# Kernel optimization log

Measured on AMD Instinct MI355X. Metric: run time of the kernel, lower is better.

The kernel has to match this reference:

```python
import jax, jax.numpy as jnp
import numpy as np

V, E, H, R, RD = 32000, 300, 300, 50, 50  # vocab, word-emb, hidden, rel vocab, rel emb
B, N = 32, 128                            # trees per batch, nodes per tree


def setup_inputs() -> dict:
    key = jax.random.key(0)
    ks = jax.random.split(key, 10)
    root_hidden = jax.random.normal(ks[0], (B, H), jnp.float32)
    relations = jax.random.randint(ks[1], (B, N), 0, R, jnp.int32)
    prev_words = jax.random.randint(ks[2], (B, N), 0, V, jnp.int32)
    # topologically sorted parent pointers: parent[i] in [-1, i-1]; -1 = virtual root
    rng = np.random.default_rng(0)
    parents = np.full((B, N), -1, dtype=np.int32)
    for i in range(1, N):
        parents[:, i] = rng.integers(-1, i, size=B)
    parents = jnp.asarray(parents)
    s_in = 1.0 / np.float32(np.sqrt(RD + E))
    s_h = 1.0 / np.float32(np.sqrt(H))
    emb = jax.random.normal(ks[3], (V, E), jnp.float32) * 0.02
    rel_emb = jax.random.normal(ks[4], (R, RD), jnp.float32) * 0.02
    W_ih = jax.random.normal(ks[5], (4 * H, RD + E), jnp.float32) * s_in
    W_hh = jax.random.normal(ks[6], (4 * H, H), jnp.float32) * s_h
    b_ih = jnp.zeros((4 * H,), jnp.float32)
    b_hh = jnp.zeros((4 * H,), jnp.float32)
    W_out = jax.random.normal(ks[7], (V, H), jnp.float32) * s_h
    b_out = jnp.zeros((V,), jnp.float32)
    return {"root_hidden": root_hidden, "relations": relations, "prev_words": prev_words,
            "parents": parents, "emb": emb, "rel_emb": rel_emb, "W_ih": W_ih, "W_hh": W_hh,
            "b_ih": b_ih, "b_hh": b_hh, "W_out": W_out, "b_out": b_out}


def reference(root_hidden, relations, prev_words, parents, emb, rel_emb,
              W_ih, W_hh, b_ih, b_hh, W_out, b_out):
    # per-node input: rel embedding ++ (teacher-forced) previous word embedding
    x = jnp.concatenate([rel_emb[relations], emb[prev_words]], axis=-1)  # [B,N,RD+E]
    xg = jnp.einsum('bni,gi->bng', x, W_ih) + b_ih                       # [B,N,4H]

    def one_tree(h0, xg_t, pars):
        n = pars.shape[0]
        h_buf = jnp.zeros((n + 1, H), xg_t.dtype).at[0].set(h0)
        c_buf = jnp.zeros((n + 1, H), xg_t.dtype).at[0].set(h0)  # original: hidden=(h,h)

        def step(carry, inp):
            hb, cb = carry
            xg_i, par, idx = inp
            ph = hb[par + 1]
            pc = cb[par + 1]
            gates = xg_i + ph @ W_hh.T + b_hh
            i_g, f_g, g_g, o_g = jnp.split(gates, 4)
            c = jax.nn.sigmoid(f_g) * pc + jax.nn.sigmoid(i_g) * jnp.tanh(g_g)
            h = jax.nn.sigmoid(o_g) * jnp.tanh(c)
            return (hb.at[idx + 1].set(h), cb.at[idx + 1].set(c)), h

        _, hs = jax.lax.scan(step, (h_buf, c_buf), (xg_t, pars, jnp.arange(n)))
        return hs  # [N,H]

    hs = jax.vmap(one_tree)(root_hidden, xg, parents)          # [B,N,H]
    logits = jnp.einsum('bnh,vh->bnv', hs, W_out) + b_out      # [B,N,V]
    return logits
```

## Files before the change

### kernel.cpp

```cpp
#include <hip/hip_runtime.h>
#include <hip/hip_bf16.h>

typedef unsigned short u16;
typedef unsigned int u32;
typedef unsigned long long u64;
typedef __attribute__((ext_vector_type(8))) short short8;
typedef __attribute__((ext_vector_type(4))) float f32x4;

#define NB 32
#define NN 128
#define HH 300
#define NV 32000
#define KP 320
#define KX 352
#define XGS 1280

#define NSLICE 15
#define UPS 20
#define NROWS 80
#define TPBS 320
#define GMAXN 16
#define LDW 328

#define A_LD(p)     __hip_atomic_load((p), __ATOMIC_RELAXED, __HIP_MEMORY_SCOPE_AGENT)
#define A_ST(p, v)  __hip_atomic_store((p), (v), __ATOMIC_RELAXED, __HIP_MEMORY_SCOPE_AGENT)
#define A_ADD(p, v) __hip_atomic_fetch_add((p), (v), __ATOMIC_RELAXED, __HIP_MEMORY_SCOPE_AGENT)

__device__ __forceinline__ float sigm(float x) { return 1.f / (1.f + __expf(-x)); }
__device__ __forceinline__ float tanh_f(float x) {
    float e = __expf(2.f * x);
    return 1.f - 2.f / (e + 1.f);
}
__device__ __forceinline__ u16 f2bf(float f) {
    __hip_bfloat16 b = __float2bfloat16(f);
    return *reinterpret_cast<u16*>(&b);
}

__global__ void k_init(const float* __restrict__ rh, u16* __restrict__ hb16,
                       int* __restrict__ lvl_done) {
    const int stride = gridDim.x * blockDim.x;
    const int idx = blockIdx.x * blockDim.x + threadIdx.x;
    for (int e = idx; e < NB * 129 * 20; e += stride) {
        int row = e / 20, c = 300 + (e - row * 20);
        hb16[(size_t)row * KP + c] = 0;
    }
    for (int e = idx; e < NB * HH; e += stride) {
        int b = e / HH, u = e - b * HH;
        hb16[(size_t)(b * 129) * KP + u] = f2bf(rh[e]);
    }
    for (int e = idx; e < NB * NN; e += stride) lvl_done[e] = 0;
}

__global__ void k_pack(const float* __restrict__ W_ih, const float* __restrict__ W_hh,
                       u16* __restrict__ Wihp, u16* __restrict__ Wp16) {
    const int tot = 1280 * KX + NSLICE * NROWS * LDW;
    for (int n = blockIdx.x * blockDim.x + threadIdx.x; n < tot; n += gridDim.x * blockDim.x) {
        if (n < 1280 * KX) {
            int r = n / KX, k = n - r * KX;
            float v = (r < 1200 && k < 350) ? W_ih[r * 350 + k] : 0.f;
            Wihp[n] = f2bf(v);
        } else {
            int m = n - 1280 * KX;
            int s = m / (NROWS * LDW);
            int rem = m - s * (NROWS * LDW);
            int r = rem / LDW, k = rem - r * LDW;
            int g = r / UPS, ul = r - g * UPS;
            int grow = g * HH + s * UPS + ul;
            float v = (k < HH) ? W_hh[grow * HH + k] : 0.f;
            Wp16[m] = f2bf(v);
        }
    }
}

__global__ void k_gatherX(const int* __restrict__ relations, const int* __restrict__ prev_words,
                          const float* __restrict__ rel_emb, const float* __restrict__ emb,
                          u16* __restrict__ X) {
    for (int e = blockIdx.x * blockDim.x + threadIdx.x; e < NB * NN * KX;
         e += gridDim.x * blockDim.x) {
        int node = e / KX, c = e - node * KX;
        float v = 0.f;
        if (c < 50) v = rel_emb[relations[node] * 50 + c];
        else if (c < 350) v = emb[(size_t)prev_words[node] * 300 + (c - 50)];
        X[e] = f2bf(v);
    }
}

__global__ void k_prep(const int* __restrict__ parents, int* __restrict__ lvl_nodes,
                       int* __restrict__ lvl_cnt, int* __restrict__ lvl_start,
                       int* __restrict__ nlev) {
    __shared__ int dep[NB][NN];
    __shared__ int cnt[NB][NN];
    __shared__ int st[NB][NN];
    const int t = threadIdx.x;
    if (t < NB) {
        for (int l = 0; l < NN; ++l) cnt[t][l] = 0;
        int md = 0;
        for (int i = 0; i < NN; ++i) {
            int p = parents[t * NN + i];
            int d = (p < 0) ? 0 : dep[t][p] + 1;
            dep[t][i] = d;
            cnt[t][d]++;
            md = max(md, d);
        }
        nlev[t] = md + 1;
        int run = 0;
        for (int l = 0; l < NN; ++l) {
            st[t][l] = run;
            lvl_start[t * NN + l] = run;
            lvl_cnt[t * NN + l] = cnt[t][l];
            run += cnt[t][l];
        }
        for (int i = 0; i < NN; ++i) {
            int d = dep[t][i];
            lvl_nodes[t * NN + st[t][d]] = i;
            st[t][d]++;
        }
    }
}

__global__ __launch_bounds__(256) void k_xgemm(const u16* __restrict__ Xbf,
                                               const u16* __restrict__ Wihp,
                                               const float* __restrict__ b_ih,
                                               float* __restrict__ xg) {
    __shared__ __align__(16) u16 As[128 * 40];
    __shared__ __align__(16) u16 Bs[128 * 40];
    const int tid = threadIdx.x;
    const int lane = tid & 63, wv = tid >> 6;
    const int wm = wv >> 1, wn = wv & 1;
    const int mblk = blockIdx.x, nblk = blockIdx.y;
    const u16* Ag = Xbf + (size_t)mblk * 128 * KX;
    const u16* Bg = Wihp + (size_t)nblk * 128 * KX;
    f32x4 acc[4][4] = {};
    const int lrow = lane & 15, lseg = lane >> 4;
    for (int kk = 0; kk < KX; kk += 32) {
#pragma unroll
        for (int q = 0; q < 2; ++q) {
            int s = tid + q * 256;
            int r = s >> 2, seg = s & 3;
            *(uint4*)&As[r * 40 + seg * 8] = *(const uint4*)&Ag[(size_t)r * KX + kk + seg * 8];
            *(uint4*)&Bs[r * 40 + seg * 8] = *(const uint4*)&Bg[(size_t)r * KX + kk + seg * 8];
        }
        __syncthreads();
        short8 av[4], bv[4];
#pragma unroll
        for (int i = 0; i < 4; ++i) {
            av[i] = *(const short8*)&As[(wm * 64 + i * 16 + lrow) * 40 + lseg * 8];
            bv[i] = *(const short8*)&Bs[(wn * 64 + i * 16 + lrow) * 40 + lseg * 8];
        }
#pragma unroll
        for (int i = 0; i < 4; ++i)
#pragma unroll
            for (int j = 0; j < 4; ++j)
                acc[i][j] = __builtin_amdgcn_mfma_f32_16x16x32_bf16(bv[j], av[i], acc[i][j],
                                                                    0, 0, 0);
        __syncthreads();
    }
#pragma unroll
    for (int i = 0; i < 4; ++i) {
        const int row = mblk * 128 + wm * 64 + i * 16 + lrow;
        float* orow = xg + (size_t)row * XGS;
#pragma unroll
        for (int j = 0; j < 4; ++j) {
            const int col = nblk * 128 + wn * 64 + j * 16 + lseg * 4;
            f32x4 v = acc[i][j];
            if (col < 1200) {
                f32x4 bo = *(const f32x4*)&b_ih[col];
                v[0] += bo[0]; v[1] += bo[1]; v[2] += bo[2]; v[3] += bo[3];
            }
            *(f32x4*)&orow[col] = v;
        }
    }
}

__global__ __launch_bounds__(TPBS) void k_scan(const int* __restrict__ parents,
                                               const u16* __restrict__ Wp16,
                                               const float* __restrict__ xg,
                                               const float* __restrict__ b_hh,
                                               const float* __restrict__ rh,
                                               u16* __restrict__ hb16,
                                               const int* __restrict__ lvl_nodes,
                                               const int* __restrict__ lvl_cnt,
                                               const int* __restrict__ lvl_start,
                                               const int* __restrict__ nlev,
                                               int* __restrict__ lvl_done) {
    __shared__ __align__(16) u16 Wl[NROWS * LDW];
    __shared__ __align__(16) u16 hs[GMAXN * LDW];
    __shared__ __align__(16) float gates[GMAXN * 82];
    __shared__ float c_lds[129 * UPS];
    __shared__ int nid_s[GMAXN], par_s[GMAXN];

    const int t = threadIdx.x;
    const int b = blockIdx.x / NSLICE;
    const int s = blockIdx.x % NSLICE;
    const int lane = t & 63, wv = t >> 6;
    const int lrow = lane & 15, lk = lane >> 4;

    {
        const u64* src = (const u64*)(Wp16 + (size_t)s * NROWS * LDW);
        u64* dst = (u64*)Wl;
        for (int e = t; e < NROWS * LDW / 4; e += TPBS) dst[e] = src[e];
    }
    if (t < UPS) c_lds[t] = rh[b * HH + s * UPS + t];
    __syncthreads();

    const int nl = nlev[b];
    for (int l = 0; l < nl; ++l) {
        const int cnt = lvl_cnt[b * NN + l];
        const int start = lvl_start[b * NN + l];
        for (int off = 0; off < cnt; off += GMAXN) {
            const int gc = min(GMAXN, cnt - off);
            if (t < gc) {
                int i = lvl_nodes[b * NN + start + off + t];
                nid_s[t] = i;
                par_s[t] = parents[b * NN + i];
            }
            __syncthreads();
            for (int e = t; e < gc * 80; e += TPBS) {
                const int j = e / 80, q = e - j * 80;
                const u64* hrow = (const u64*)(hb16 +
                    (size_t)(b * 129 + par_s[j] + 1) * KP);
                *(u64*)&hs[j * LDW + q * 4] = A_LD(&hrow[q]);
            }
            __syncthreads();
            {
                f32x4 acc = {};
#pragma unroll
                for (int kk = 0; kk < KP; kk += 32) {
                    short8 av = *(const short8*)&hs[lrow * LDW + kk + lk * 8];
                    short8 bv = *(const short8*)&Wl[(wv * 16 + lrow) * LDW + kk + lk * 8];
                    acc = __builtin_amdgcn_mfma_f32_16x16x32_bf16(av, bv, acc, 0, 0, 0);
                }
#pragma unroll
                for (int r = 0; r < 4; ++r)
                    gates[(lk * 4 + r) * 82 + wv * 16 + lrow] = acc[r];
            }
            __syncthreads();
            if (t < 160) {
                const int j = t / 10, up = t - j * 10;
                if (j < gc) {
                    const int i = nid_s[j];
                    const int par = par_s[j];
                    const int ul0 = up * 2;
                    const float* gj = gates + j * 82;
                    const float* xgp = xg + (size_t)(b * NN + i) * XGS + s * UPS;
                    const float* bhp = b_hh + s * UPS;
                    float hv[2];
#pragma unroll
                    for (int un = 0; un < 2; ++un) {
                        const int ul = ul0 + un;
                        float gs[4];
#pragma unroll
                        for (int g = 0; g < 4; ++g)
                            gs[g] = gj[g * UPS + ul] + xgp[g * HH + ul] + bhp[g * HH + ul];
                        const float pc = c_lds[(par + 1) * UPS + ul];
                        const float cv = sigm(gs[1]) * pc + sigm(gs[0]) * tanh_f(gs[2]);
                        hv[un] = sigm(gs[3]) * tanh_f(cv);
                        c_lds[(i + 1) * UPS + ul] = cv;
                    }
                    const u32 hp = (u32)f2bf(hv[0]) | ((u32)f2bf(hv[1]) << 16);
                    A_ST((u32*)(hb16 + (size_t)(b * 129 + i + 1) * KP + s * UPS + ul0), hp);
                }
            }
            __syncthreads();
        }
        if (l + 1 < nl) {
            if (t == 0) {
                int* dp = &lvl_done[b * NN + l];
                const int old = A_ADD(dp, 1);
                if (old != NSLICE - 1) {
                    while (A_LD(dp) < NSLICE) __builtin_amdgcn_s_sleep(1);
                }
            }
            __syncthreads();
        }
    }
}

__global__ void k_cast_B(const float* __restrict__ W_out, u16* __restrict__ Bm) {
    for (int e = blockIdx.x * blockDim.x + threadIdx.x; e < NV * KP;
         e += gridDim.x * blockDim.x) {
        int v = e / KP, k = e - v * KP;
        float x = (k < HH) ? W_out[v * HH + k] : 0.f;
        Bm[e] = f2bf(x);
    }
}

__global__ __launch_bounds__(256) void k_gemm(const u16* __restrict__ hb16,
                                              const u16* __restrict__ Bbf,
                                              const float* __restrict__ b_out,
                                              float* __restrict__ out) {
    __shared__ __align__(16) u16 As[128 * 40];
    __shared__ __align__(16) u16 Bs[128 * 40];
    const int tid = threadIdx.x;
    const int lane = tid & 63, wv = tid >> 6;
    const int wm = wv >> 1, wn = wv & 1;
    const int bid = blockIdx.x;
    const int newbid = (bid & 7) * 1000 + (bid >> 3);
    const int mblk = newbid & 31, nblk = newbid >> 5;
    const u16* Ag = hb16 + ((size_t)mblk * 129 + 1) * KP;
    const u16* Bg = Bbf + (size_t)nblk * 128 * KP;
    f32x4 acc[4][4] = {};
    const int lrow = lane & 15, lseg = lane >> 4;
    for (int kk = 0; kk < KP; kk += 32) {
#pragma unroll
        for (int q = 0; q < 2; ++q) {
            int s = tid + q * 256;
            int r = s >> 2, seg = s & 3;
            *(uint4*)&As[r * 40 + seg * 8] = *(const uint4*)&Ag[r * KP + kk + seg * 8];
            *(uint4*)&Bs[r * 40 + seg * 8] = *(const uint4*)&Bg[r * KP + kk + seg * 8];
        }
        __syncthreads();
        short8 av[4], bv[4];
#pragma unroll
        for (int i = 0; i < 4; ++i) {
            av[i] = *(const short8*)&As[(wm * 64 + i * 16 + lrow) * 40 + lseg * 8];
            bv[i] = *(const short8*)&Bs[(wn * 64 + i * 16 + lrow) * 40 + lseg * 8];
        }
#pragma unroll
        for (int i = 0; i < 4; ++i)
#pragma unroll
            for (int j = 0; j < 4; ++j)
                acc[i][j] = __builtin_amdgcn_mfma_f32_16x16x32_bf16(bv[j], av[i], acc[i][j],
                                                                    0, 0, 0);
        __syncthreads();
    }
#pragma unroll
    for (int i = 0; i < 4; ++i) {
        const int row = mblk * 128 + wm * 64 + i * 16 + lrow;
        float* orow = out + (size_t)row * NV;
#pragma unroll
        for (int j = 0; j < 4; ++j) {
            const int col = nblk * 128 + wn * 64 + j * 16 + lseg * 4;
            f32x4 v = acc[i][j];
            f32x4 bo = *(const f32x4*)&b_out[col];
            v[0] += bo[0]; v[1] += bo[1]; v[2] += bo[2]; v[3] += bo[3];
            __builtin_nontemporal_store(v, (f32x4*)&orow[col]);
        }
    }
}

extern "C" void kernel_launch(void* const* d_in, const int* in_sizes, int n_in,
                              void* d_out, int out_size, void* d_ws, size_t ws_size,
                              hipStream_t stream) {
    const float* root_hidden = (const float*)d_in[0];
    const int* relations = (const int*)d_in[1];
    const int* prev_words = (const int*)d_in[2];
    const int* parents = (const int*)d_in[3];
    const float* emb = (const float*)d_in[4];
    const float* rel_emb = (const float*)d_in[5];
    const float* W_ih = (const float*)d_in[6];
    const float* W_hh = (const float*)d_in[7];
    const float* b_ih = (const float*)d_in[8];
    const float* b_hh = (const float*)d_in[9];
    const float* W_out = (const float*)d_in[10];
    const float* b_out = (const float*)d_in[11];
    float* out = (float*)d_out;

    float* xg = (float*)d_ws;
    u16* Xbf = (u16*)(xg + 4096 * XGS);
    u16* Wihp = Xbf + 4096 * KX;
    u16* Wp16 = Wihp + 1280 * KX;
    u16* hb16 = Wp16 + NSLICE * NROWS * LDW;
    u16* Bbf = hb16 + 1320960;
    int* lvl_nodes = (int*)(Bbf + 10240000);
    int* lvl_cnt = lvl_nodes + 4096;
    int* lvl_start = lvl_cnt + 4096;
    int* nlev = lvl_start + 4096;
    int* lvl_done = nlev + 64;

    k_init<<<128, 256, 0, stream>>>(root_hidden, hb16, lvl_done);
    k_pack<<<1024, 256, 0, stream>>>(W_ih, W_hh, Wihp, Wp16);
    k_gatherX<<<1024, 256, 0, stream>>>(relations, prev_words, rel_emb, emb, Xbf);
    k_prep<<<1, 64, 0, stream>>>(parents, lvl_nodes, lvl_cnt, lvl_start, nlev);

    k_xgemm<<<dim3(32, 10), 256, 0, stream>>>(Xbf, Wihp, b_ih, xg);

    k_scan<<<dim3(NB * NSLICE), dim3(TPBS), 0, stream>>>(
        parents, Wp16, xg, b_hh, root_hidden, hb16,
        lvl_nodes, lvl_cnt, lvl_start, nlev, lvl_done);

    k_cast_B<<<4096, 256, 0, stream>>>(W_out, Bbf);
    k_gemm<<<dim3(8000), 256, 0, stream>>>(hb16, Bbf, b_out, out);
}
```

Baseline: 341.7 us.

## Fuse prelude kernels and use direct global-to-LDS loads in logits GEMM

Merges init, weight packing, embedding gather and W_out bf16 cast into one prelude kernel, removing three launches and moving the W_out cast before the scan. The W_out cast now writes four bf16 values per store. The output GEMM stages A/B tiles with global_load_lds (direct global-to-LDS) into an XOR-swizzled unpadded LDS layout instead of register round-trip copies, aiming to cut VGPR traffic and bank conflicts. The swizzle must match the MFMA read pattern, and the GEMM still has no double buffering.

```diff
diff --git a/kernel.cpp b/kernel.cpp
--- a/kernel.cpp
+++ b/kernel.cpp
@@ -35,9 +35,26 @@
     __hip_bfloat16 b = __float2bfloat16(f);
     return *reinterpret_cast<u16*>(&b);
 }
-
-__global__ void k_init(const float* __restrict__ rh, u16* __restrict__ hb16,
-                       int* __restrict__ lvl_done) {
+__device__ __forceinline__ void gl_lds16(const u16* gsrc, u16* ldst) {
+    __builtin_amdgcn_global_load_lds(
+        (const __attribute__((address_space(1))) void*)gsrc,
+        (__attribute__((address_space(3))) void*)ldst, 16, 0, 0);
+}
+
+__global__ __launch_bounds__(256) void k_prelude(const float* __restrict__ rh,
+                                                 const int* __restrict__ relations,
+                                                 const int* __restrict__ prev_words,
+                                                 const float* __restrict__ rel_emb,
+                                                 const float* __restrict__ emb,
+                                                 const float* __restrict__ W_ih,
+                                                 const float* __restrict__ W_hh,
+                                                 const float* __restrict__ W_out,
+                                                 u16* __restrict__ hb16,
+                                                 int* __restrict__ lvl_done,
+                                                 u16* __restrict__ Wihp,
+                                                 u16* __restrict__ Wp16,
+                                                 u16* __restrict__ Xbf,
+                                                 u16* __restrict__ Bbf) {
     const int stride = gridDim.x * blockDim.x;
     const int idx = blockIdx.x * blockDim.x + threadIdx.x;
     for (int e = idx; e < NB * 129 * 20; e += stride) {
@@ -49,39 +66,38 @@
         hb16[(size_t)(b * 129) * KP + u] = f2bf(rh[e]);
     }
     for (int e = idx; e < NB * NN; e += stride) lvl_done[e] = 0;
-}
-
-__global__ void k_pack(const float* __restrict__ W_ih, const float* __restrict__ W_hh,
-                       u16* __restrict__ Wihp, u16* __restrict__ Wp16) {
-    const int tot = 1280 * KX + NSLICE * NROWS * LDW;
-    for (int n = blockIdx.x * blockDim.x + threadIdx.x; n < tot; n += gridDim.x * blockDim.x) {
-        if (n < 1280 * KX) {
-            int r = n / KX, k = n - r * KX;
-            float v = (r < 1200 && k < 350) ? W_ih[r * 350 + k] : 0.f;
-            Wihp[n] = f2bf(v);
-        } else {
-            int m = n - 1280 * KX;
-            int s = m / (NROWS * LDW);
-            int rem = m - s * (NROWS * LDW);
-            int r = rem / LDW, k = rem - r * LDW;
-            int g = r / UPS, ul = r - g * UPS;
-            int grow = g * HH + s * UPS + ul;
-            float v = (k < HH) ? W_hh[grow * HH + k] : 0.f;
-            Wp16[m] = f2bf(v);
-        }
-    }
-}
-
-__global__ void k_gatherX(const int* __restrict__ relations, const int* __restrict__ prev_words,
-                          const float* __restrict__ rel_emb, const float* __restrict__ emb,
-                          u16* __restrict__ X) {
-    for (int e = blockIdx.x * blockDim.x + threadIdx.x; e < NB * NN * KX;
-         e += gridDim.x * blockDim.x) {
+    for (int n = idx; n < 1280 * KX; n += stride) {
+        int r = n / KX, k = n - r * KX;
+        float v = (r < 1200 && k < 350) ? W_ih[r * 350 + k] : 0.f;
+        Wihp[n] = f2bf(v);
+    }
+    for (int m = idx; m < NSLICE * NROWS * LDW; m += stride) {
+        int s = m / (NROWS * LDW);
+        int rem = m - s * (NROWS * LDW);
+        int r = rem / LDW, k = rem - r * LDW;
+        int g = r / UPS, ul = r - g * UPS;
+        int grow = g * HH + s * UPS + ul;
+        float v = (k < HH) ? W_hh[grow * HH + k] : 0.f;
+        Wp16[m] = f2bf(v);
+    }
+    for (int e = idx; e < NB * NN * KX; e += stride) {
         int node = e / KX, c = e - node * KX;
         float v = 0.f;
         if (c < 50) v = rel_emb[relations[node] * 50 + c];
         else if (c < 350) v = emb[(size_t)prev_words[node] * 300 + (c - 50)];
-        X[e] = f2bf(v);
+        Xbf[e] = f2bf(v);
+    }
+    u64* Bq = (u64*)Bbf;
+    for (int e = idx; e < NV * KP / 4; e += stride) {
+        const int c4 = e * 4;
+        const int v = c4 / KP, k = c4 - v * KP;
+        const float* wr = W_out + (size_t)v * HH;
+        float x0 = (k + 0 < HH) ? wr[k + 0] : 0.f;
+        float x1 = (k + 1 < HH) ? wr[k + 1] : 0.f;
+        float x2 = (k + 2 < HH) ? wr[k + 2] : 0.f;
+        float x3 = (k + 3 < HH) ? wr[k + 3] : 0.f;
+        Bq[e] = (u64)f2bf(x0) | ((u64)f2bf(x1) << 16) |
+                ((u64)f2bf(x2) << 32) | ((u64)f2bf(x3) << 48);
     }
 }
 
@@ -276,21 +292,12 @@
     }
 }
 
-__global__ void k_cast_B(const float* __restrict__ W_out, u16* __restrict__ Bm) {
-    for (int e = blockIdx.x * blockDim.x + threadIdx.x; e < NV * KP;
-         e += gridDim.x * blockDim.x) {
-        int v = e / KP, k = e - v * KP;
-        float x = (k < HH) ? W_out[v * HH + k] : 0.f;
-        Bm[e] = f2bf(x);
-    }
-}
-
 __global__ __launch_bounds__(256) void k_gemm(const u16* __restrict__ hb16,
                                               const u16* __restrict__ Bbf,
                                               const float* __restrict__ b_out,
                                               float* __restrict__ out) {
-    __shared__ __align__(16) u16 As[128 * 40];
-    __shared__ __align__(16) u16 Bs[128 * 40];
+    __shared__ __align__(16) u16 As[128 * 32];
+    __shared__ __align__(16) u16 Bs[128 * 32];
     const int tid = threadIdx.x;
     const int lane = tid & 63, wv = tid >> 6;
     const int wm = wv >> 1, wn = wv & 1;
@@ -299,22 +306,32 @@
     const int mblk = newbid & 31, nblk = newbid >> 5;
     const u16* Ag = hb16 + ((size_t)mblk * 129 + 1) * KP;
     const u16* Bg = Bbf + (size_t)nblk * 128 * KP;
+    const int r0 = wv * 32 + (lane >> 2);
+    const int r1 = r0 + 16;
+    const int q0 = lane & 3;
+    const int lk0 = (q0 - (r0 >> 1)) & 3;
+    const int lk1 = (q0 - (r1 >> 1)) & 3;
+    const u16* pa0 = Ag + (size_t)r0 * KP + lk0 * 8;
+    const u16* pa1 = Ag + (size_t)r1 * KP + lk1 * 8;
+    const u16* pb0 = Bg + (size_t)r0 * KP + lk0 * 8;
+    const u16* pb1 = Bg + (size_t)r1 * KP + lk1 * 8;
+    u16* lA = As + wv * 1024;
+    u16* lB = Bs + wv * 1024;
     f32x4 acc[4][4] = {};
     const int lrow = lane & 15, lseg = lane >> 4;
     for (int kk = 0; kk < KP; kk += 32) {
-#pragma unroll
-        for (int q = 0; q < 2; ++q) {
-            int s = tid + q * 256;
-            int r = s >> 2, seg = s & 3;
-            *(uint4*)&As[r * 40 + seg * 8] = *(const uint4*)&Ag[r * KP + kk + seg * 8];
-            *(uint4*)&Bs[r * 40 + seg * 8] = *(const uint4*)&Bg[r * KP + kk + seg * 8];
-        }
+        gl_lds16(pa0 + kk, lA);
+        gl_lds16(pa1 + kk, lA + 512);
+        gl_lds16(pb0 + kk, lB);
+        gl_lds16(pb1 + kk, lB + 512);
         __syncthreads();
         short8 av[4], bv[4];
 #pragma unroll
         for (int i = 0; i < 4; ++i) {
-            av[i] = *(const short8*)&As[(wm * 64 + i * 16 + lrow) * 40 + lseg * 8];
-            bv[i] = *(const short8*)&Bs[(wn * 64 + i * 16 + lrow) * 40 + lseg * 8];
+            const int ra = wm * 64 + i * 16 + lrow;
+            const int rb = wn * 64 + i * 16 + lrow;
+            av[i] = *(const short8*)&As[ra * 32 + (((lseg + (ra >> 1)) & 3) * 8)];
+            bv[i] = *(const short8*)&Bs[rb * 32 + (((lseg + (rb >> 1)) & 3) * 8)];
         }
 #pragma unroll
         for (int i = 0; i < 4; ++i)
@@ -368,9 +385,9 @@
     int* nlev = lvl_start + 4096;
     int* lvl_done = nlev + 64;
 
-    k_init<<<128, 256, 0, stream>>>(root_hidden, hb16, lvl_done);
-    k_pack<<<1024, 256, 0, stream>>>(W_ih, W_hh, Wihp, Wp16);
-    k_gatherX<<<1024, 256, 0, stream>>>(relations, prev_words, rel_emb, emb, Xbf);
+    k_prelude<<<2048, 256, 0, stream>>>(root_hidden, relations, prev_words, rel_emb, emb,
+                                        W_ih, W_hh, W_out, hb16, lvl_done, Wihp, Wp16,
+                                        Xbf, Bbf);
     k_prep<<<1, 64, 0, stream>>>(parents, lvl_nodes, lvl_cnt, lvl_start, nlev);
 
     k_xgemm<<<dim3(32, 10), 256, 0, stream>>>(Xbf, Wihp, b_ih, xg);
@@ -379,6 +396,5 @@
         parents, Wp16, xg, b_hh, root_hidden, hb16,
         lvl_nodes, lvl_cnt, lvl_start, nlev, lvl_done);
 
-    k_cast_B<<<4096, 256, 0, stream>>>(W_out, Bbf);
     k_gemm<<<dim3(8000), 256, 0, stream>>>(hb16, Bbf, b_out, out);
 }
```

Measured after the change: 328.4 us, median of 2. 3.9% less time.
